# Optimization experiments

Hardware: AMD Instinct MI355X
Metric: run time of the kernel (lower is better)

The kernel has to match this reference:

```python
import jax, jax.numpy as jnp
import numpy as np

N, E, D, G, L = 100000, 1600000, 32, 64, 3
BN_EPS = 1e-5


def setup_inputs() -> dict:
    key = jax.random.key(0)
    ks = jax.random.split(key, 8)
    x = jax.random.normal(ks[0], (N, D), dtype=jnp.float32)
    edge_index = jax.random.randint(ks[1], (2, E), 0, N, dtype=jnp.int64)
    batch = jnp.sort(jax.random.randint(ks[2], (N,), 0, G, dtype=jnp.int64))
    layer_weights = jnp.ones((L,), dtype=jnp.float32)
    # linears[i]: Linear(D->D) + BN(D) (inference-mode stats) ; L of them
    lin_W = jax.random.normal(ks[3], (L, D, D), dtype=jnp.float32) * (1.0 / np.sqrt(D))
    lin_b = jnp.zeros((L, D), dtype=jnp.float32)
    lin_gamma = jnp.ones((L, D), dtype=jnp.float32)
    lin_beta = jnp.zeros((L, D), dtype=jnp.float32)
    lin_mean = jnp.zeros((L, D), dtype=jnp.float32)
    lin_var = jnp.ones((L, D), dtype=jnp.float32)
    # GINConv MLPs: Linear(D->D) + BN(D) + ELU ; L-1 of them
    conv_W = jax.random.normal(ks[4], (L - 1, D, D), dtype=jnp.float32) * (1.0 / np.sqrt(D))
    conv_b = jnp.zeros((L - 1, D), dtype=jnp.float32)
    conv_gamma = jnp.ones((L - 1, D), dtype=jnp.float32)
    conv_beta = jnp.zeros((L - 1, D), dtype=jnp.float32)
    conv_mean = jnp.zeros((L - 1, D), dtype=jnp.float32)
    conv_var = jnp.ones((L - 1, D), dtype=jnp.float32)
    return {"x": x, "edge_index": edge_index, "batch": batch,
            "layer_weights": layer_weights,
            "lin_W": lin_W, "lin_b": lin_b, "lin_gamma": lin_gamma,
            "lin_beta": lin_beta, "lin_mean": lin_mean, "lin_var": lin_var,
            "conv_W": conv_W, "conv_b": conv_b, "conv_gamma": conv_gamma,
            "conv_beta": conv_beta, "conv_mean": conv_mean, "conv_var": conv_var}


def _mlp(h, W, b, gamma, beta, mean, var):
    # Linear -> BatchNorm1d (inference stats) -> ELU
    h = h @ W + b
    h = (h - mean) * (gamma * jax.lax.rsqrt(var + BN_EPS)) + beta
    return jax.nn.elu(h)


def reference(x, edge_index, batch, layer_weights,
              lin_W, lin_b, lin_gamma, lin_beta, lin_mean, lin_var,
              conv_W, conv_b, conv_gamma, conv_beta, conv_mean, conv_var):
    src, dst = edge_index[0], edge_index[1]
    z = _mlp(x, lin_W[0], lin_b[0], lin_gamma[0], lin_beta[0], lin_mean[0], lin_var[0])
    Z = layer_weights[0] * z
    out = jax.ops.segment_max(z, batch, num_segments=G)  # global_max_pool
    for l in range(1, L):
        # GINConv (eps=0): x' = MLP(x + sum_{j->i} x_j)
        agg = jax.ops.segment_sum(x[src], dst, num_segments=N)
        x = _mlp(x + agg, conv_W[l - 1], conv_b[l - 1], conv_gamma[l - 1],
                 conv_beta[l - 1], conv_mean[l - 1], conv_var[l - 1])
        z = layer_weights[l] * _mlp(x, lin_W[l], lin_b[l], lin_gamma[l],
                                    lin_beta[l], lin_mean[l], lin_var[l])
        Z = Z + z
        out = out + jax.ops.segment_max(z, batch, num_segments=G)
    # dropout p=0.0 is identity
    return (out, Z, x)
```

## Files before the change

kernel.cpp:

```cpp
#include <hip/hip_runtime.h>
#include <math.h>

#define N_NODES 100000
#define N_EDGES 1600000
#define DIM 32
#define N_GROUPS 64
#define BN_EPS 1e-5f

#define BIN_NODES 128
#define NBINS ((N_NODES + BIN_NODES - 1) / BIN_NODES)
#define EPB_HIST 8192
#define HIST_BLOCKS ((N_EDGES + EPB_HIST - 1) / EPB_HIST)

#define HLS 40

typedef __attribute__((ext_vector_type(8))) short short8;
typedef __attribute__((ext_vector_type(4))) float f32x4;

__device__ __forceinline__ unsigned enc_f32(float f) {
    unsigned u = __float_as_uint(f);
    return (u & 0x80000000u) ? ~u : (u | 0x80000000u);
}
__device__ __forceinline__ float dec_f32(unsigned u) {
    return (u & 0x80000000u) ? __uint_as_float(u & 0x7FFFFFFFu) : __uint_as_float(~u);
}
__device__ __forceinline__ unsigned short f2bf(float f) {
    unsigned u = __float_as_uint(f);
    u += 0x7FFFu + ((u >> 16) & 1u);
    return (unsigned short)(u >> 16);
}

__global__ void fold_kernel(const float* __restrict__ lin_W, const float* __restrict__ lin_b,
                            const float* __restrict__ lin_gamma, const float* __restrict__ lin_beta,
                            const float* __restrict__ lin_mean, const float* __restrict__ lin_var,
                            const float* __restrict__ conv_W, const float* __restrict__ conv_b,
                            const float* __restrict__ conv_gamma, const float* __restrict__ conv_beta,
                            const float* __restrict__ conv_mean, const float* __restrict__ conv_var,
                            float* __restrict__ Wf, float* __restrict__ shf,
                            unsigned short* __restrict__ Wfb,
                            float* __restrict__ out, unsigned* __restrict__ segmx,
                            int* __restrict__ bincnt)
{
    int l = blockIdx.x;
    int t = threadIdx.x;
    if (l == 5) {
        out[t] = 0.f; out[t + 1024] = 0.f;
        segmx[t] = 0; segmx[t + 1024] = 0;
        if (t < NBINS) bincnt[t] = 0;
        return;
    }
    const float *W, *b, *gm, *bt, *mn, *vr;
    if (l < 3) {
        W = lin_W + l * DIM * DIM; b = lin_b + l * DIM; gm = lin_gamma + l * DIM;
        bt = lin_beta + l * DIM;   mn = lin_mean + l * DIM; vr = lin_var + l * DIM;
    } else {
        int c = l - 3;
        W = conv_W + c * DIM * DIM; b = conv_b + c * DIM; gm = conv_gamma + c * DIM;
        bt = conv_beta + c * DIM;   mn = conv_mean + c * DIM; vr = conv_var + c * DIM;
    }
    int j = t & (DIM - 1);
    float scale = gm[j] / sqrtf(vr[j] + BN_EPS);
    float w = W[t] * scale;
    Wf[l * DIM * DIM + t] = w;
    Wfb[l * DIM * DIM + t] = f2bf(w);
    if (t < DIM) shf[l * DIM + t] = (b[t] - mn[t]) * scale + bt[t];
}

__global__ __launch_bounds__(256) void binhist_kernel(const int* __restrict__ dst,
                                                      int* __restrict__ bincnt,
                                                      int* __restrict__ blockcnt) {
    __shared__ int cnt[NBINS];
    int t = threadIdx.x;
    for (int b = t; b < NBINS; b += 256) cnt[b] = 0;
    __syncthreads();
    int base = blockIdx.x * EPB_HIST;
    for (int i = 0; i < EPB_HIST / 256; ++i) {
        int e = base + i * 256 + t;
        if (e < N_EDGES) atomicAdd(&cnt[dst[e] >> 7], 1);
    }
    __syncthreads();
    for (int b = t; b < NBINS; b += 256) {
        int c = cnt[b];
        blockcnt[(size_t)blockIdx.x * NBINS + b] = c;
        if (c > 0) atomicAdd(&bincnt[b], c);
    }
}

__global__ __launch_bounds__(1024) void binscan_kernel(const int* __restrict__ bincnt,
                                                       int* __restrict__ binoff,
                                                       int* __restrict__ bincur) {
    __shared__ int s[1024];
    int t = threadIdx.x;
    int c = (t < NBINS) ? bincnt[t] : 0;
    s[t] = c;
    __syncthreads();
    for (int off = 1; off < 1024; off <<= 1) {
        int u = (t >= off) ? s[t - off] : 0;
        __syncthreads();
        s[t] += u;
        __syncthreads();
    }
    if (t < NBINS) { binoff[t] = s[t] - c; bincur[t] = s[t] - c; }
    if (t == 0) binoff[NBINS] = N_EDGES;
}

__global__ __launch_bounds__(256) void binscatter_kernel(const int* __restrict__ src,
                                                         const int* __restrict__ dst,
                                                         int* __restrict__ bincur,
                                                         unsigned* __restrict__ binbuf,
                                                         const int* __restrict__ blockcnt) {
    __shared__ int pos[NBINS];
    int t = threadIdx.x;
    for (int b = t; b < NBINS; b += 256) {
        int c = blockcnt[(size_t)blockIdx.x * NBINS + b];
        pos[b] = (c > 0) ? atomicAdd(&bincur[b], c) : 0;
    }
    __syncthreads();
    int base = blockIdx.x * EPB_HIST;
    for (int i = 0; i < EPB_HIST / 256; ++i) {
        int e = base + i * 256 + t;
        if (e < N_EDGES) {
            int d = dst[e];
            int bin = d >> 7;
            int p = atomicAdd(&pos[bin], 1);
            binbuf[p] = ((unsigned)(d & 127) << 17) | (unsigned)src[e];
        }
    }
}

__global__ __launch_bounds__(256) void binsort_kernel(const unsigned* __restrict__ binbuf,
                                                      const int* __restrict__ binoff,
                                                      int* __restrict__ esrc,
                                                      int* __restrict__ nodeptr) {
    __shared__ int cnt[BIN_NODES];
    __shared__ int sc[BIN_NODES];
    int t = threadIdx.x;
    int bin = blockIdx.x;
    int beg = binoff[bin], end = binoff[bin + 1];
    if (t < BIN_NODES) cnt[t] = 0;
    __syncthreads();
    for (int e = beg + t; e < end; e += 256)
        atomicAdd(&cnt[binbuf[e] >> 17], 1);
    __syncthreads();
    int v = (t < BIN_NODES) ? cnt[t] : 0;
    if (t < BIN_NODES) sc[t] = v;
    __syncthreads();
    for (int off = 1; off < BIN_NODES; off <<= 1) {
        int u = (t < BIN_NODES && t >= off) ? sc[t - off] : 0;
        __syncthreads();
        if (t < BIN_NODES) sc[t] += u;
        __syncthreads();
    }
    if (t < BIN_NODES) {
        int excl = sc[t] - v;
        cnt[t] = excl;
        nodeptr[bin * BIN_NODES + t] = beg + excl;
    }
    __syncthreads();
    for (int e = beg + t; e < end; e += 256) {
        unsigned pe = binbuf[e];
        int dl = (int)(pe >> 17);
        int p = atomicAdd(&cnt[dl], 1);
        esrc[beg + p] = (int)(pe & 0x1FFFFu);
    }
}

__global__ __launch_bounds__(256) void gin_fused_kernel(
        const unsigned short* __restrict__ xb,
        const int* __restrict__ esrc,
        const int* __restrict__ nodeptr,
        const unsigned short* __restrict__ Wcb, const float* __restrict__ shc,
        const unsigned short* __restrict__ Wlb, const float* __restrict__ shl,
        const int* __restrict__ batch, const float* __restrict__ lw_ptr,
        unsigned short* __restrict__ xnextb,
        float* __restrict__ xoutf,
        float* __restrict__ Z,
        unsigned* __restrict__ segmax)
{
    __shared__ __align__(16) unsigned short hl[4][16 * HLS];
    __shared__ unsigned segloc[8 * DIM];
    int t = threadIdx.x;
    segloc[t] = 0;

    int wv = t >> 6, lane = t & 63;
    int m = lane & 15, kg = lane >> 4;

    short8 bc0, bc1, bl0, bl1;
#pragma unroll
    for (int j = 0; j < 8; ++j) {
        int k = kg * 8 + j;
        bc0[j] = (short)Wcb[k * DIM + m];
        bc1[j] = (short)Wcb[k * DIM + 16 + m];
        bl0[j] = (short)Wlb[k * DIM + m];
        bl1[j] = (short)Wlb[k * DIM + 16 + m];
    }
    float shc0 = shc[m], shc1 = shc[m + 16];
    float shl0 = shl[m], shl1 = shl[m + 16];
    float lw = lw_ptr[0];
    int blk0 = blockIdx.x * 64;
    int gfirst = batch[blk0 < N_NODES ? blk0 : N_NODES - 1];
    int row0 = blk0 + wv * 16;
    __syncthreads();

    if (row0 < N_NODES) {
        int beg = nodeptr[row0 + m];
        int deg = nodeptr[row0 + m + 1] - beg;
        int md = deg;
#pragma unroll
        for (int off = 1; off < 16; off <<= 1)
            md = max(md, __shfl_xor(md, off, 64));

        short8 aA = *(const short8*)(xb + (size_t)(row0 + m) * DIM + kg * 8);
        f32x4 d0a = {0.f, 0.f, 0.f, 0.f}, d1a = {0.f, 0.f, 0.f, 0.f};
        f32x4 d0b = {0.f, 0.f, 0.f, 0.f}, d1b = {0.f, 0.f, 0.f, 0.f};
        d0a = __builtin_amdgcn_mfma_f32_16x16x32_bf16(aA, bc0, d0a, 0, 0, 0);
        d1a = __builtin_amdgcn_mfma_f32_16x16x32_bf16(aA, bc1, d1a, 0, 0, 0);

        int i = 0;
        for (; i + 1 < md; i += 2) {
            short8 a0 = {0, 0, 0, 0, 0, 0, 0, 0};
            short8 a1 = {0, 0, 0, 0, 0, 0, 0, 0};
            if (i < deg) {
                int s = esrc[beg + i];
                a0 = *(const short8*)(xb + (size_t)s * DIM + kg * 8);
            }
            if (i + 1 < deg) {
                int s = esrc[beg + i + 1];
                a1 = *(const short8*)(xb + (size_t)s * DIM + kg * 8);
            }
            d0a = __builtin_amdgcn_mfma_f32_16x16x32_bf16(a0, bc0, d0a, 0, 0, 0);
            d1a = __builtin_amdgcn_mfma_f32_16x16x32_bf16(a0, bc1, d1a, 0, 0, 0);
            d0b = __builtin_amdgcn_mfma_f32_16x16x32_bf16(a1, bc0, d0b, 0, 0, 0);
            d1b = __builtin_amdgcn_mfma_f32_16x16x32_bf16(a1, bc1, d1b, 0, 0, 0);
        }
        if (i < md) {
            short8 a0 = {0, 0, 0, 0, 0, 0, 0, 0};
            if (i < deg) {
                int s = esrc[beg + i];
                a0 = *(const short8*)(xb + (size_t)s * DIM + kg * 8);
            }
            d0a = __builtin_amdgcn_mfma_f32_16x16x32_bf16(a0, bc0, d0a, 0, 0, 0);
            d1a = __builtin_amdgcn_mfma_f32_16x16x32_bf16(a0, bc1, d1a, 0, 0, 0);
        }

        float hp0[4], hp1[4];
#pragma unroll
        for (int r = 0; r < 4; ++r) {
            float a0 = d0a[r] + d0b[r] + shc0;
            float a1 = d1a[r] + d1b[r] + shc1;
            hp0[r] = a0 > 0.f ? a0 : expm1f(a0);
            hp1[r] = a1 > 0.f ? a1 : expm1f(a1);
        }
#pragma unroll
        for (int r = 0; r < 4; ++r) {
            hl[wv][(kg * 4 + r) * HLS + m] = f2bf(hp0[r]);
            hl[wv][(kg * 4 + r) * HLS + 16 + m] = f2bf(hp1[r]);
        }
        if (xoutf) {
#pragma unroll
            for (int r = 0; r < 4; ++r) {
                int row = row0 + kg * 4 + r;
                xoutf[(size_t)row * DIM + m] = hp0[r];
                xoutf[(size_t)row * DIM + 16 + m] = hp1[r];
            }
        }
        if (xnextb) {
            int ii = lane >> 2, q = lane & 3;
            uint4 pk = *(const uint4*)&hl[wv][ii * HLS + q * 8];
            *(uint4*)(xnextb + (size_t)(row0 + ii) * DIM + q * 8) = pk;
        }

        short8 a2 = *(const short8*)&hl[wv][m * HLS + kg * 8];
        f32x4 e0 = {0.f, 0.f, 0.f, 0.f}, e1 = {0.f, 0.f, 0.f, 0.f};
        e0 = __builtin_amdgcn_mfma_f32_16x16x32_bf16(a2, bl0, e0, 0, 0, 0);
        e1 = __builtin_amdgcn_mfma_f32_16x16x32_bf16(a2, bl1, e1, 0, 0, 0);
#pragma unroll
        for (int r = 0; r < 4; ++r) {
            int row = row0 + kg * 4 + r;
            float a0 = e0[r] + shl0, a1 = e1[r] + shl1;
            float z0 = a0 > 0.f ? a0 : expm1f(a0);
            float z1 = a1 > 0.f ? a1 : expm1f(a1);
            float zw0 = lw * z0, zw1 = lw * z1;
            size_t zi = (size_t)row * DIM;
            Z[zi + m] += zw0;
            Z[zi + 16 + m] += zw1;
            int g = batch[row];
            int go = g - gfirst;
            if (go < 8) {
                atomicMax(&segloc[go * DIM + m], enc_f32(zw0));
                atomicMax(&segloc[go * DIM + 16 + m], enc_f32(zw1));
            } else {
                atomicMax(&segmax[g * DIM + m], enc_f32(zw0));
                atomicMax(&segmax[g * DIM + 16 + m], enc_f32(zw1));
            }
        }
    }
    __syncthreads();
    unsigned v = segloc[t];
    if (v) atomicMax(&segmax[(gfirst + (t >> 5)) * DIM + (t & 31)], v);
}

__global__ __launch_bounds__(256) void linZ_first_kernel(
        const float* __restrict__ x0,
        unsigned short* __restrict__ x0b,
        const unsigned short* __restrict__ Wb,
        const float* __restrict__ shf,
        const int* __restrict__ batch,
        const float* __restrict__ lw_ptr,
        float* __restrict__ Z,
        unsigned* __restrict__ segmax)
{
    __shared__ unsigned segloc[8 * DIM];
    int t = threadIdx.x;
    segloc[t] = 0;

    int wv = t >> 6, lane = t & 63;
    int m = lane & 15, kg = lane >> 4;

    short8 b0, b1;
#pragma unroll
    for (int j = 0; j < 8; ++j) {
        int k = kg * 8 + j;
        b0[j] = (short)Wb[k * DIM + m];
        b1[j] = (short)Wb[k * DIM + 16 + m];
    }
    float sh0 = shf[m], sh1 = shf[m + 16];
    float lw = lw_ptr[0];
    int blk0 = blockIdx.x * 64;
    int gfirst = batch[blk0 < N_NODES ? blk0 : N_NODES - 1];
    int row0 = blk0 + wv * 16;
    __syncthreads();

    if (row0 < N_NODES) {
        const float* rp = x0 + (size_t)(row0 + m) * DIM + kg * 8;
        float4 v0 = *(const float4*)rp;
        float4 v1 = *(const float4*)(rp + 4);
        short8 a;
        a[0] = (short)f2bf(v0.x); a[1] = (short)f2bf(v0.y);
        a[2] = (short)f2bf(v0.z); a[3] = (short)f2bf(v0.w);
        a[4] = (short)f2bf(v1.x); a[5] = (short)f2bf(v1.y);
        a[6] = (short)f2bf(v1.z); a[7] = (short)f2bf(v1.w);
        *(short8*)(x0b + (size_t)(row0 + m) * DIM + kg * 8) = a;

        f32x4 d0 = {0.f, 0.f, 0.f, 0.f}, d1 = {0.f, 0.f, 0.f, 0.f};
        d0 = __builtin_amdgcn_mfma_f32_16x16x32_bf16(a, b0, d0, 0, 0, 0);
        d1 = __builtin_amdgcn_mfma_f32_16x16x32_bf16(a, b1, d1, 0, 0, 0);
#pragma unroll
        for (int r = 0; r < 4; ++r) {
            int row = row0 + kg * 4 + r;
            float a0 = d0[r] + sh0;
            float a1 = d1[r] + sh1;
            float z0 = a0 > 0.f ? a0 : expm1f(a0);
            float z1 = a1 > 0.f ? a1 : expm1f(a1);
            size_t zi = (size_t)row * DIM;
            Z[zi + m] = lw * z0;
            Z[zi + 16 + m] = lw * z1;
            int g = batch[row];
            int go = g - gfirst;
            if (go < 8) {
                atomicMax(&segloc[go * DIM + m], enc_f32(z0));
                atomicMax(&segloc[go * DIM + 16 + m], enc_f32(z1));
            } else {
                atomicMax(&segmax[g * DIM + m], enc_f32(z0));
                atomicMax(&segmax[g * DIM + 16 + m], enc_f32(z1));
            }
        }
    }
    __syncthreads();
    unsigned v = segloc[t];
    if (v) atomicMax(&segmax[(gfirst + (t >> 5)) * DIM + (t & 31)], v);
}

__global__ void add_out_kernel(unsigned* __restrict__ segmax, float* __restrict__ out) {
    int t = blockIdx.x * blockDim.x + threadIdx.x;
    out[t] += dec_f32(segmax[t]);
    segmax[t] = 0;
}

extern "C" void kernel_launch(void* const* d_in, const int* in_sizes, int n_in,
                              void* d_out, int out_size, void* d_ws, size_t ws_size,
                              hipStream_t stream) {
    const float* x0        = (const float*)d_in[0];
    const int*   ei        = (const int*)d_in[1];
    const int*   batch     = (const int*)d_in[2];
    const float* lw        = (const float*)d_in[3];
    const float* lin_W     = (const float*)d_in[4];
    const float* lin_b     = (const float*)d_in[5];
    const float* lin_gamma = (const float*)d_in[6];
    const float* lin_beta  = (const float*)d_in[7];
    const float* lin_mean  = (const float*)d_in[8];
    const float* lin_var   = (const float*)d_in[9];
    const float* conv_W    = (const float*)d_in[10];
    const float* conv_b    = (const float*)d_in[11];
    const float* conv_gamma= (const float*)d_in[12];
    const float* conv_beta = (const float*)d_in[13];
    const float* conv_mean = (const float*)d_in[14];
    const float* conv_var  = (const float*)d_in[15];

    float* out  = (float*)d_out;
    float* Z    = out + N_GROUPS * DIM;
    float* xout = Z + (size_t)N_NODES * DIM;

    char* p = (char*)d_ws;
    unsigned short* x0b     = (unsigned short*)p; p += ((size_t)N_NODES * DIM + 8192) * sizeof(unsigned short);
    unsigned short* xbufb   = (unsigned short*)p; p += ((size_t)N_NODES * DIM + 8192) * sizeof(unsigned short);
    unsigned*       binbuf  = (unsigned*)p;       p += (size_t)N_EDGES * sizeof(unsigned);
    int*            esrc    = (int*)p;            p += (size_t)N_EDGES * sizeof(int);
    int*            nodeptr = (int*)p;            p += (NBINS * BIN_NODES + 1) * sizeof(int);
    int*            blockcnt= (int*)p;            p += (size_t)HIST_BLOCKS * NBINS * sizeof(int);
    int*            bincnt  = (int*)p;            p += NBINS * sizeof(int);
    int*            binoff  = (int*)p;            p += (NBINS + 1) * sizeof(int);
    int*            bincur  = (int*)p;            p += NBINS * sizeof(int);
    unsigned*       segmx   = (unsigned*)p;       p += N_GROUPS * DIM * sizeof(unsigned);
    float*          Wf      = (float*)p;          p += 5 * DIM * DIM * sizeof(float);
    float*          shf     = (float*)p;          p += 5 * DIM * sizeof(float);
    unsigned short* Wfb     = (unsigned short*)p; p += 5 * DIM * DIM * sizeof(unsigned short);

    const int* src = ei;
    const int* dst = ei + N_EDGES;

    const int gf_blocks = (N_NODES + 63) / 64;

    fold_kernel<<<6, 1024, 0, stream>>>(lin_W, lin_b, lin_gamma, lin_beta, lin_mean, lin_var,
                                        conv_W, conv_b, conv_gamma, conv_beta, conv_mean, conv_var,
                                        Wf, shf, Wfb, out, segmx, bincnt);

    binhist_kernel<<<HIST_BLOCKS, 256, 0, stream>>>(dst, bincnt, blockcnt);
    binscan_kernel<<<1, 1024, 0, stream>>>(bincnt, binoff, bincur);
    binscatter_kernel<<<HIST_BLOCKS, 256, 0, stream>>>(src, dst, bincur, binbuf, blockcnt);
    binsort_kernel<<<NBINS, 256, 0, stream>>>(binbuf, binoff, esrc, nodeptr);

    linZ_first_kernel<<<gf_blocks, 256, 0, stream>>>(x0, x0b, Wfb, shf, batch, lw, Z, segmx);
    add_out_kernel<<<8, 256, 0, stream>>>(segmx, out);

    gin_fused_kernel<<<gf_blocks, 256, 0, stream>>>(x0b, esrc, nodeptr,
                                                    Wfb + 3 * DIM * DIM, shf + 3 * DIM,
                                                    Wfb + 1 * DIM * DIM, shf + 1 * DIM,
                                                    batch, lw + 1,
                                                    xbufb, (float*)nullptr, Z, segmx);
    add_out_kernel<<<8, 256, 0, stream>>>(segmx, out);

    gin_fused_kernel<<<gf_blocks, 256, 0, stream>>>(xbufb, esrc, nodeptr,
                                                    Wfb + 4 * DIM * DIM, shf + 4 * DIM,
                                                    Wfb + 2 * DIM * DIM, shf + 2 * DIM,
                                                    batch, lw + 2,
                                                    (unsigned short*)nullptr, xout, Z, segmx);
    add_out_kernel<<<8, 256, 0, stream>>>(segmx, out);
}
```

Before: 258.4 us.

## Fuse edge scatter with first linear layer and deepen gather pipelining

Merges the bin-scatter kernel with the first-layer linear/Z kernel into one launch, and folds the segment-max accumulation into the bin-sort launch as extra blocks, removing two launches. Pads the global bin counters to separate cache lines, shrinks edges per histogram block for more parallelism, and reuses the xbufb workspace for block counts. The GIN gather loop now fetches four neighbor rows per step with double-buffered prefetch, clamps out-of-range indices to a zeroed sentinel row instead of branching, and spreads the sum over four accumulators. This increases register pressure, and reusing xbufb for block counts relies on its contents not being needed until later.

After: 287.2 us. +11.1%, slower.

```diff
diff --git a/kernel.cpp b/kernel.cpp
--- a/kernel.cpp
+++ b/kernel.cpp
@@ -9,8 +9,9 @@
 
 #define BIN_NODES 128
 #define NBINS ((N_NODES + BIN_NODES - 1) / BIN_NODES)
-#define EPB_HIST 8192
+#define EPB_HIST 2048
 #define HIST_BLOCKS ((N_EDGES + EPB_HIST - 1) / EPB_HIST)
+#define CNT_PAD 16
 
 #define HLS 40
 
@@ -39,14 +40,20 @@
                             float* __restrict__ Wf, float* __restrict__ shf,
                             unsigned short* __restrict__ Wfb,
                             float* __restrict__ out, unsigned* __restrict__ segmx,
-                            int* __restrict__ bincnt)
+                            int* __restrict__ bincnt,
+                            unsigned short* __restrict__ x0b,
+                            unsigned short* __restrict__ xbufb)
 {
     int l = blockIdx.x;
     int t = threadIdx.x;
     if (l == 5) {
         out[t] = 0.f; out[t + 1024] = 0.f;
         segmx[t] = 0; segmx[t + 1024] = 0;
-        if (t < NBINS) bincnt[t] = 0;
+        for (int z = t; z < NBINS * CNT_PAD; z += 1024) bincnt[z] = 0;
+        if (t < DIM) {
+            x0b[(size_t)N_NODES * DIM + t] = 0;
+            xbufb[(size_t)N_NODES * DIM + t] = 0;
+        }
         return;
     }
     const float *W, *b, *gm, *bt, *mn, *vr;
@@ -82,7 +89,7 @@
     for (int b = t; b < NBINS; b += 256) {
         int c = cnt[b];
         blockcnt[(size_t)blockIdx.x * NBINS + b] = c;
-        if (c > 0) atomicAdd(&bincnt[b], c);
+        if (c > 0) atomicAdd(&bincnt[b * CNT_PAD], c);
     }
 }
 
@@ -91,7 +98,7 @@
                                                        int* __restrict__ bincur) {
     __shared__ int s[1024];
     int t = threadIdx.x;
-    int c = (t < NBINS) ? bincnt[t] : 0;
+    int c = (t < NBINS) ? bincnt[t * CNT_PAD] : 0;
     s[t] = c;
     __syncthreads();
     for (int off = 1; off < 1024; off <<= 1) {
@@ -100,41 +107,117 @@
         s[t] += u;
         __syncthreads();
     }
-    if (t < NBINS) { binoff[t] = s[t] - c; bincur[t] = s[t] - c; }
+    if (t < NBINS) { binoff[t] = s[t] - c; bincur[t * CNT_PAD] = s[t] - c; }
     if (t == 0) binoff[NBINS] = N_EDGES;
 }
 
-__global__ __launch_bounds__(256) void binscatter_kernel(const int* __restrict__ src,
-                                                         const int* __restrict__ dst,
-                                                         int* __restrict__ bincur,
-                                                         unsigned* __restrict__ binbuf,
-                                                         const int* __restrict__ blockcnt) {
-    __shared__ int pos[NBINS];
-    int t = threadIdx.x;
-    for (int b = t; b < NBINS; b += 256) {
-        int c = blockcnt[(size_t)blockIdx.x * NBINS + b];
-        pos[b] = (c > 0) ? atomicAdd(&bincur[b], c) : 0;
-    }
-    __syncthreads();
-    int base = blockIdx.x * EPB_HIST;
-    for (int i = 0; i < EPB_HIST / 256; ++i) {
-        int e = base + i * 256 + t;
-        if (e < N_EDGES) {
-            int d = dst[e];
-            int bin = d >> 7;
-            int p = atomicAdd(&pos[bin], 1);
-            binbuf[p] = ((unsigned)(d & 127) << 17) | (unsigned)src[e];
-        }
-    }
+__global__ __launch_bounds__(256) void scatter_linz_kernel(
+        const int* __restrict__ src, const int* __restrict__ dst,
+        int* __restrict__ bincur, unsigned* __restrict__ binbuf,
+        const int* __restrict__ blockcnt,
+        const float* __restrict__ x0, unsigned short* __restrict__ x0b,
+        const unsigned short* __restrict__ Wb, const float* __restrict__ shfv,
+        const int* __restrict__ batch, const float* __restrict__ lw_ptr,
+        float* __restrict__ Z, unsigned* __restrict__ segmax)
+{
+    __shared__ int smem[NBINS];
+    int t = threadIdx.x;
+
+    if (blockIdx.x < HIST_BLOCKS) {
+        int* pos = smem;
+        for (int b = t; b < NBINS; b += 256) {
+            int c = blockcnt[(size_t)blockIdx.x * NBINS + b];
+            pos[b] = (c > 0) ? atomicAdd(&bincur[b * CNT_PAD], c) : 0;
+        }
+        __syncthreads();
+        int base = blockIdx.x * EPB_HIST;
+        for (int i = 0; i < EPB_HIST / 256; ++i) {
+            int e = base + i * 256 + t;
+            if (e < N_EDGES) {
+                int d = dst[e];
+                int bin = d >> 7;
+                int p = atomicAdd(&pos[bin], 1);
+                binbuf[p] = ((unsigned)(d & 127) << 17) | (unsigned)src[e];
+            }
+        }
+        return;
+    }
+
+    unsigned* segloc = (unsigned*)smem;
+    segloc[t] = 0;
+
+    int wv = t >> 6, lane = t & 63;
+    int m = lane & 15, kg = lane >> 4;
+
+    short8 b0, b1;
+#pragma unroll
+    for (int j = 0; j < 8; ++j) {
+        int k = kg * 8 + j;
+        b0[j] = (short)Wb[k * DIM + m];
+        b1[j] = (short)Wb[k * DIM + 16 + m];
+    }
+    float sh0 = shfv[m], sh1 = shfv[m + 16];
+    float lw = lw_ptr[0];
+    int blk0 = (blockIdx.x - HIST_BLOCKS) * 64;
+    int gfirst = batch[blk0 < N_NODES ? blk0 : N_NODES - 1];
+    int row0 = blk0 + wv * 16;
+    __syncthreads();
+
+    if (row0 < N_NODES) {
+        const float* rp = x0 + (size_t)(row0 + m) * DIM + kg * 8;
+        float4 v0 = *(const float4*)rp;
+        float4 v1 = *(const float4*)(rp + 4);
+        short8 a;
+        a[0] = (short)f2bf(v0.x); a[1] = (short)f2bf(v0.y);
+        a[2] = (short)f2bf(v0.z); a[3] = (short)f2bf(v0.w);
+        a[4] = (short)f2bf(v1.x); a[5] = (short)f2bf(v1.y);
+        a[6] = (short)f2bf(v1.z); a[7] = (short)f2bf(v1.w);
+        *(short8*)(x0b + (size_t)(row0 + m) * DIM + kg * 8) = a;
+
+        f32x4 d0 = {0.f, 0.f, 0.f, 0.f}, d1 = {0.f, 0.f, 0.f, 0.f};
+        d0 = __builtin_amdgcn_mfma_f32_16x16x32_bf16(a, b0, d0, 0, 0, 0);
+        d1 = __builtin_amdgcn_mfma_f32_16x16x32_bf16(a, b1, d1, 0, 0, 0);
+#pragma unroll
+        for (int r = 0; r < 4; ++r) {
+            int row = row0 + kg * 4 + r;
+            float a0 = d0[r] + sh0;
+            float a1 = d1[r] + sh1;
+            float z0 = a0 > 0.f ? a0 : expm1f(a0);
+            float z1 = a1 > 0.f ? a1 : expm1f(a1);
+            size_t zi = (size_t)row * DIM;
+            Z[zi + m] = lw * z0;
+            Z[zi + 16 + m] = lw * z1;
+            int g = batch[row];
+            int go = g - gfirst;
+            if (go < 8) {
+                atomicMax(&segloc[go * DIM + m], enc_f32(z0));
+                atomicMax(&segloc[go * DIM + 16 + m], enc_f32(z1));
+            } else {
+                atomicMax(&segmax[g * DIM + m], enc_f32(z0));
+                atomicMax(&segmax[g * DIM + 16 + m], enc_f32(z1));
+            }
+        }
+    }
+    __syncthreads();
+    unsigned v = segloc[t];
+    if (v) atomicMax(&segmax[(gfirst + (t >> 5)) * DIM + (t & 31)], v);
 }
 
 __global__ __launch_bounds__(256) void binsort_kernel(const unsigned* __restrict__ binbuf,
                                                       const int* __restrict__ binoff,
                                                       int* __restrict__ esrc,
-                                                      int* __restrict__ nodeptr) {
+                                                      int* __restrict__ nodeptr,
+                                                      unsigned* __restrict__ segmax,
+                                                      float* __restrict__ out) {
+    int t = threadIdx.x;
+    if (blockIdx.x >= NBINS) {
+        int t2 = (blockIdx.x - NBINS) * 256 + t;
+        out[t2] += dec_f32(segmax[t2]);
+        segmax[t2] = 0;
+        return;
+    }
     __shared__ int cnt[BIN_NODES];
     __shared__ int sc[BIN_NODES];
-    int t = threadIdx.x;
     int bin = blockIdx.x;
     int beg = binoff[bin], end = binoff[bin + 1];
     if (t < BIN_NODES) cnt[t] = 0;
@@ -164,6 +247,28 @@
         esrc[beg + p] = (int)(pe & 0x1FFFFu);
     }
 }
+
+#define GIN_FETCH4(I0, A)                                                       \
+  {                                                                             \
+    _Pragma("unroll")                                                           \
+    for (int q_ = 0; q_ < 4; ++q_) {                                            \
+      int ii_ = (I0) + q_;                                                      \
+      int ei_ = beg + ii_;                                                      \
+      ei_ = ei_ < (N_EDGES - 1) ? ei_ : (N_EDGES - 1);                          \
+      int s_ = esrc[ei_];                                                       \
+      s_ = (ii_ < deg) ? s_ : N_NODES;                                          \
+      A[q_] = *(const short8*)(xb + (size_t)s_ * DIM + kg8);                    \
+    }                                                                           \
+  }
+
+#define GIN_MFMA4(A)                                                            \
+  {                                                                             \
+    _Pragma("unroll")                                                           \
+    for (int q_ = 0; q_ < 4; ++q_) {                                            \
+      d0[q_] = __builtin_amdgcn_mfma_f32_16x16x32_bf16(A[q_], bc0, d0[q_], 0, 0, 0); \
+      d1[q_] = __builtin_amdgcn_mfma_f32_16x16x32_bf16(A[q_], bc1, d1[q_], 0, 0, 0); \
+    }                                                                           \
+  }
 
 __global__ __launch_bounds__(256) void gin_fused_kernel(
         const unsigned short* __restrict__ xb,
@@ -184,11 +289,12 @@
 
     int wv = t >> 6, lane = t & 63;
     int m = lane & 15, kg = lane >> 4;
+    int kg8 = kg * 8;
 
     short8 bc0, bc1, bl0, bl1;
 #pragma unroll
     for (int j = 0; j < 8; ++j) {
-        int k = kg * 8 + j;
+        int k = kg8 + j;
         bc0[j] = (short)Wcb[k * DIM + m];
         bc1[j] = (short)Wcb[k * DIM + 16 + m];
         bl0[j] = (short)Wlb[k * DIM + m];
@@ -210,44 +316,41 @@
         for (int off = 1; off < 16; off <<= 1)
             md = max(md, __shfl_xor(md, off, 64));
 
-        short8 aA = *(const short8*)(xb + (size_t)(row0 + m) * DIM + kg * 8);
-        f32x4 d0a = {0.f, 0.f, 0.f, 0.f}, d1a = {0.f, 0.f, 0.f, 0.f};
-        f32x4 d0b = {0.f, 0.f, 0.f, 0.f}, d1b = {0.f, 0.f, 0.f, 0.f};
-        d0a = __builtin_amdgcn_mfma_f32_16x16x32_bf16(aA, bc0, d0a, 0, 0, 0);
-        d1a = __builtin_amdgcn_mfma_f32_16x16x32_bf16(aA, bc1, d1a, 0, 0, 0);
-
-        int i = 0;
-        for (; i + 1 < md; i += 2) {
-            short8 a0 = {0, 0, 0, 0, 0, 0, 0, 0};
-            short8 a1 = {0, 0, 0, 0, 0, 0, 0, 0};
-            if (i < deg) {
-                int s = esrc[beg + i];
-                a0 = *(const short8*)(xb + (size_t)s * DIM + kg * 8);
-            }
-            if (i + 1 < deg) {
-                int s = esrc[beg + i + 1];
-                a1 = *(const short8*)(xb + (size_t)s * DIM + kg * 8);
-            }
-            d0a = __builtin_amdgcn_mfma_f32_16x16x32_bf16(a0, bc0, d0a, 0, 0, 0);
-            d1a = __builtin_amdgcn_mfma_f32_16x16x32_bf16(a0, bc1, d1a, 0, 0, 0);
-            d0b = __builtin_amdgcn_mfma_f32_16x16x32_bf16(a1, bc0, d0b, 0, 0, 0);
-            d1b = __builtin_amdgcn_mfma_f32_16x16x32_bf16(a1, bc1, d1b, 0, 0, 0);
-        }
-        if (i < md) {
-            short8 a0 = {0, 0, 0, 0, 0, 0, 0, 0};
-            if (i < deg) {
-                int s = esrc[beg + i];
-                a0 = *(const short8*)(xb + (size_t)s * DIM + kg * 8);
-            }
-            d0a = __builtin_amdgcn_mfma_f32_16x16x32_bf16(a0, bc0, d0a, 0, 0, 0);
-            d1a = __builtin_amdgcn_mfma_f32_16x16x32_bf16(a0, bc1, d1a, 0, 0, 0);
+        short8 aS = *(const short8*)(xb + (size_t)(row0 + m) * DIM + kg8);
+        f32x4 d0[4], d1[4];
+#pragma unroll
+        for (int q = 0; q < 4; ++q) {
+            d0[q] = (f32x4){0.f, 0.f, 0.f, 0.f};
+            d1[q] = (f32x4){0.f, 0.f, 0.f, 0.f};
+        }
+        d0[0] = __builtin_amdgcn_mfma_f32_16x16x32_bf16(aS, bc0, d0[0], 0, 0, 0);
+        d1[0] = __builtin_amdgcn_mfma_f32_16x16x32_bf16(aS, bc1, d1[0], 0, 0, 0);
+
+        int B = (md + 3) >> 2;
+        if (B > 0) {
+            short8 aA[4], aB[4];
+            GIN_FETCH4(0, aA);
+            int k = 1;
+            for (; k + 1 < B; k += 2) {
+                GIN_FETCH4(4 * k, aB);
+                GIN_MFMA4(aA);
+                GIN_FETCH4(4 * (k + 1), aA);
+                GIN_MFMA4(aB);
+            }
+            if (k < B) {
+                GIN_FETCH4(4 * k, aB);
+                GIN_MFMA4(aA);
+                GIN_MFMA4(aB);
+            } else {
+                GIN_MFMA4(aA);
+            }
         }
 
         float hp0[4], hp1[4];
 #pragma unroll
         for (int r = 0; r < 4; ++r) {
-            float a0 = d0a[r] + d0b[r] + shc0;
-            float a1 = d1a[r] + d1b[r] + shc1;
+            float a0 = d0[0][r] + d0[1][r] + d0[2][r] + d0[3][r] + shc0;
+            float a1 = d1[0][r] + d1[1][r] + d1[2][r] + d1[3][r] + shc1;
             hp0[r] = a0 > 0.f ? a0 : expm1f(a0);
             hp1[r] = a1 > 0.f ? a1 : expm1f(a1);
         }
@@ -270,7 +373,7 @@
             *(uint4*)(xnextb + (size_t)(row0 + ii) * DIM + q * 8) = pk;
         }
 
-        short8 a2 = *(const short8*)&hl[wv][m * HLS + kg * 8];
+        short8 a2 = *(const short8*)&hl[wv][m * HLS + kg8];
         f32x4 e0 = {0.f, 0.f, 0.f, 0.f}, e1 = {0.f, 0.f, 0.f, 0.f};
         e0 = __builtin_amdgcn_mfma_f32_16x16x32_bf16(a2, bl0, e0, 0, 0, 0);
         e1 = __builtin_amdgcn_mfma_f32_16x16x32_bf16(a2, bl1, e1, 0, 0, 0);
@@ -292,77 +395,6 @@
             } else {
                 atomicMax(&segmax[g * DIM + m], enc_f32(zw0));
                 atomicMax(&segmax[g * DIM + 16 + m], enc_f32(zw1));
-            }
-        }
-    }
-    __syncthreads();
-    unsigned v = segloc[t];
-    if (v) atomicMax(&segmax[(gfirst + (t >> 5)) * DIM + (t & 31)], v);
-}
-
-__global__ __launch_bounds__(256) void linZ_first_kernel(
-        const float* __restrict__ x0,
-        unsigned short* __restrict__ x0b,
-        const unsigned short* __restrict__ Wb,
-        const float* __restrict__ shf,
-        const int* __restrict__ batch,
-        const float* __restrict__ lw_ptr,
-        float* __restrict__ Z,
-        unsigned* __restrict__ segmax)
-{
-    __shared__ unsigned segloc[8 * DIM];
-    int t = threadIdx.x;
-    segloc[t] = 0;
-
-    int wv = t >> 6, lane = t & 63;
-    int m = lane & 15, kg = lane >> 4;
-
-    short8 b0, b1;
-#pragma unroll
-    for (int j = 0; j < 8; ++j) {
-        int k = kg * 8 + j;
-        b0[j] = (short)Wb[k * DIM + m];
-        b1[j] = (short)Wb[k * DIM + 16 + m];
-    }
-    float sh0 = shf[m], sh1 = shf[m + 16];
-    float lw = lw_ptr[0];
-    int blk0 = blockIdx.x * 64;
-    int gfirst = batch[blk0 < N_NODES ? blk0 : N_NODES - 1];
-    int row0 = blk0 + wv * 16;
-    __syncthreads();
-
-    if (row0 < N_NODES) {
-        const float* rp = x0 + (size_t)(row0 + m) * DIM + kg * 8;
-        float4 v0 = *(const float4*)rp;
-        float4 v1 = *(const float4*)(rp + 4);
-        short8 a;
-        a[0] = (short)f2bf(v0.x); a[1] = (short)f2bf(v0.y);
-        a[2] = (short)f2bf(v0.z); a[3] = (short)f2bf(v0.w);
-        a[4] = (short)f2bf(v1.x); a[5] = (short)f2bf(v1.y);
-        a[6] = (short)f2bf(v1.z); a[7] = (short)f2bf(v1.w);
-        *(short8*)(x0b + (size_t)(row0 + m) * DIM + kg * 8) = a;
-
-        f32x4 d0 = {0.f, 0.f, 0.f, 0.f}, d1 = {0.f, 0.f, 0.f, 0.f};
-        d0 = __builtin_amdgcn_mfma_f32_16x16x32_bf16(a, b0, d0, 0, 0, 0);
-        d1 = __builtin_amdgcn_mfma_f32_16x16x32_bf16(a, b1, d1, 0, 0, 0);
-#pragma unroll
-        for (int r = 0; r < 4; ++r) {
-            int row = row0 + kg * 4 + r;
-            float a0 = d0[r] + sh0;
-            float a1 = d1[r] + sh1;
-            float z0 = a0 > 0.f ? a0 : expm1f(a0);
-            float z1 = a1 > 0.f ? a1 : expm1f(a1);
-            size_t zi = (size_t)row * DIM;
-            Z[zi + m] = lw * z0;
-            Z[zi + 16 + m] = lw * z1;
-            int g = batch[row];
-            int go = g - gfirst;
-            if (go < 8) {
-                atomicMax(&segloc[go * DIM + m], enc_f32(z0));
-                atomicMax(&segloc[go * DIM + 16 + m], enc_f32(z1));
-            } else {
-                atomicMax(&segmax[g * DIM + m], enc_f32(z0));
-                atomicMax(&segmax[g * DIM + 16 + m], enc_f32(z1));
             }
         }
     }
@@ -407,15 +439,16 @@
     unsigned*       binbuf  = (unsigned*)p;       p += (size_t)N_EDGES * sizeof(unsigned);
     int*            esrc    = (int*)p;            p += (size_t)N_EDGES * sizeof(int);
     int*            nodeptr = (int*)p;            p += (NBINS * BIN_NODES + 1) * sizeof(int);
-    int*            blockcnt= (int*)p;            p += (size_t)HIST_BLOCKS * NBINS * sizeof(int);
-    int*            bincnt  = (int*)p;            p += NBINS * sizeof(int);
+    int*            bincnt  = (int*)p;            p += NBINS * CNT_PAD * sizeof(int);
     int*            binoff  = (int*)p;            p += (NBINS + 1) * sizeof(int);
-    int*            bincur  = (int*)p;            p += NBINS * sizeof(int);
+    int*            bincur  = (int*)p;            p += NBINS * CNT_PAD * sizeof(int);
     unsigned*       segmx   = (unsigned*)p;       p += N_GROUPS * DIM * sizeof(unsigned);
     float*          Wf      = (float*)p;          p += 5 * DIM * DIM * sizeof(float);
     float*          shf     = (float*)p;          p += 5 * DIM * sizeof(float);
     unsigned short* Wfb     = (unsigned short*)p; p += 5 * DIM * DIM * sizeof(unsigned short);
 
+    int* blockcnt = (int*)xbufb;
+
     const int* src = ei;
     const int* dst = ei + N_EDGES;
 
@@ -423,15 +456,14 @@
 
     fold_kernel<<<6, 1024, 0, stream>>>(lin_W, lin_b, lin_gamma, lin_beta, lin_mean, lin_var,
                                         conv_W, conv_b, conv_gamma, conv_beta, conv_mean, conv_var,
-                                        Wf, shf, Wfb, out, segmx, bincnt);
+                                        Wf, shf, Wfb, out, segmx, bincnt, x0b, xbufb);
 
     binhist_kernel<<<HIST_BLOCKS, 256, 0, stream>>>(dst, bincnt, blockcnt);
     binscan_kernel<<<1, 1024, 0, stream>>>(bincnt, binoff, bincur);
-    binscatter_kernel<<<HIST_BLOCKS, 256, 0, stream>>>(src, dst, bincur, binbuf, blockcnt);
-    binsort_kernel<<<NBINS, 256, 0, stream>>>(binbuf, binoff, esrc, nodeptr);
-
-    linZ_first_kernel<<<gf_blocks, 256, 0, stream>>>(x0, x0b, Wfb, shf, batch, lw, Z, segmx);
-    add_out_kernel<<<8, 256, 0, stream>>>(segmx, out);
+    scatter_linz_kernel<<<HIST_BLOCKS + gf_blocks, 256, 0, stream>>>(
+        src, dst, bincur, binbuf, blockcnt,
+        x0, x0b, Wfb, shf, batch, lw, Z, segmx);
+    binsort_kernel<<<NBINS + 8, 256, 0, stream>>>(binbuf, binoff, esrc, nodeptr, segmx, out);
 
     gin_fused_kernel<<<gf_blocks, 256, 0, stream>>>(x0b, esrc, nodeptr,
                                                     Wfb + 3 * DIM * DIM, shf + 3 * DIM,
```
